# Kernel optimization log

Measured on AMD Instinct MI355X. Metric: run time of the kernel, lower is better.

Reference implementation:

```python
import jax, jax.numpy as jnp
import numpy as np

EPS = 1e-5  # torch InstanceNorm2d default eps


def setup_inputs() -> dict:
    key = jax.random.key(0)
    ks = jax.random.split(key, 5)
    B, C, H, W = 4, 64, 64, 64
    x = jax.random.normal(ks[0], (B, C, H, W), dtype=jnp.float32)
    # Conv2d 1x1 weights as [out_c, in_c] matrices (kernel dims squeezed)
    w_qkv = jax.random.normal(ks[1], (3 * C, C), dtype=jnp.float32) * (C ** -0.5)
    b_qkv = jax.random.normal(ks[2], (3 * C,), dtype=jnp.float32) * 0.02
    w_proj = jax.random.normal(ks[3], (C, C), dtype=jnp.float32) * (C ** -0.5)
    b_proj = jax.random.normal(ks[4], (C,), dtype=jnp.float32) * 0.02
    return {"x": x, "w_qkv": w_qkv, "b_qkv": b_qkv, "w_proj": w_proj, "b_proj": b_proj}


def reference(x, w_qkv, b_qkv, w_proj, b_proj):
    B, C, H, W = x.shape
    scale = C ** -0.5
    # InstanceNorm2d(affine=False): per-(B,C) stats over spatial dims, biased var
    mean = jnp.mean(x, axis=(2, 3), keepdims=True)
    var = jnp.var(x, axis=(2, 3), keepdims=True)
    h = (x - mean) * jax.lax.rsqrt(var + EPS)
    # 1x1 conv qkv projection: [B,3C,H,W]
    qkv = jnp.einsum('bchw,oc->bohw', h, w_qkv) + b_qkv[None, :, None, None]
    q, k, v = jnp.split(qkv, 3, axis=1)
    HW = H * W
    q = q.reshape(B, C, HW).transpose(0, 2, 1)  # [B, HW, C]
    k = k.reshape(B, C, HW)                      # [B, C, HW]
    v = v.reshape(B, C, HW).transpose(0, 2, 1)  # [B, HW, C]
    attn = jnp.einsum('bnc,bcm->bnm', q, k) * scale  # [B, HW, HW]
    attn = jax.nn.softmax(attn, axis=-1)
    # dropout p=0.0 -> identity
    h = jnp.einsum('bnm,bmc->bnc', attn, v)          # [B, HW, C]
    h = h.transpose(0, 2, 1).reshape(B, C, H, W)
    h = jnp.einsum('bchw,oc->bohw', h, w_proj) + b_proj[None, :, None, None]
    return x + h
```

## Files before the change

kernel.cpp:

```cpp
#include <hip/hip_runtime.h>
#include <hip/hip_bf16.h>

#define B_ 4
#define C_ 64
#define N_ 4096
#define EPS_ 1e-5f
#define C2_ 0.18033688011112042f

typedef __hip_bfloat16 bf16;
typedef __attribute__((ext_vector_type(8))) short short8;
typedef __attribute__((ext_vector_type(4))) short short4v;
typedef __attribute__((ext_vector_type(4))) float f32x4;

__device__ __forceinline__ float b2f(bf16 v) { return __bfloat162float(v); }

__device__ __forceinline__ short f2bs(float f) {
  union { bf16 h; short s; } u;
  u.h = __float2bfloat16(f);
  return u.s;
}

__device__ __forceinline__ short8 pk8(const float* f) {
  union { short8 v; short s[8]; } u;
#pragma unroll
  for (int i = 0; i < 8; ++i) u.s[i] = f2bs(f[i]);
  return u.v;
}

__device__ __forceinline__ void up8(short8 v, float* d) {
  union { short8 v; unsigned u[4]; } x;
  x.v = v;
  d[0] = __uint_as_float(x.u[0] << 16);
  d[1] = __uint_as_float(x.u[0] & 0xffff0000u);
  d[2] = __uint_as_float(x.u[1] << 16);
  d[3] = __uint_as_float(x.u[1] & 0xffff0000u);
  d[4] = __uint_as_float(x.u[2] << 16);
  d[5] = __uint_as_float(x.u[2] & 0xffff0000u);
  d[6] = __uint_as_float(x.u[3] << 16);
  d[7] = __uint_as_float(x.u[3] & 0xffff0000u);
}

template <bool F32>
__device__ __forceinline__ float ldx(const void* p, size_t idx) {
  if (F32) return ((const float*)p)[idx];
  return b2f(((const bf16*)p)[idx]);
}

template <bool F32>
__device__ __forceinline__ short8 ld8(const void* p, int idx) {
  if (F32) {
    const float* fp = (const float*)p + idx;
    float tmp[8];
    *(float4*)&tmp[0] = *(const float4*)fp;
    *(float4*)&tmp[4] = *(const float4*)(fp + 4);
    return pk8(tmp);
  }
  return *(const short8*)((const bf16*)p + idx);
}

__device__ __forceinline__ f32x4 mfma32(short8 a, short8 b, f32x4 c) {
  return __builtin_amdgcn_mfma_f32_16x16x32_bf16(a, b, c, 0, 0, 0);
}
__device__ __forceinline__ f32x4 mfma16(short4v a, short4v b, f32x4 c) {
  return __builtin_amdgcn_mfma_f32_16x16x16bf16_1k(a, b, c, 0, 0, 0);
}


template <bool F32>
__device__ __forceinline__ void stats_sum(const void* x, int bc, int t,
                                          float& s, float& s2) {
  if (F32) {
    const float4* xp = (const float4*)((const float*)x + (size_t)bc * N_);
#pragma unroll
    for (int r = 0; r < 4; ++r) {
      const float4 v = xp[r * 256 + t];
      s += (v.x + v.y) + (v.z + v.w);
      s2 += (v.x * v.x + v.y * v.y) + (v.z * v.z + v.w * v.w);
    }
  } else {
    const bf16* xp = (const bf16*)x + (size_t)bc * N_;
#pragma unroll
    for (int r = 0; r < 2; ++r) {
      float f[8];
      up8(*(const short8*)(xp + (r * 256 + t) * 8), f);
#pragma unroll
      for (int i = 0; i < 8; ++i) { s += f[i]; s2 += f[i] * f[i]; }
    }
  }
}

__global__ __launch_bounds__(256) void k_stats(const void* __restrict__ x,
                                               float* __restrict__ meanArr,
                                               float* __restrict__ rstdArr,
                                               int* __restrict__ flag) {
  const int bc = blockIdx.x, t = threadIdx.x;
  __shared__ float ps[4], ps2[4];
  __shared__ int pflag;
  {
    const ushort* xw = (const ushort*)x + (size_t)bc * 4096;
    int cnt = 0;
#pragma unroll
    for (int j = 0; j < 4; ++j) {
      const ushort4 u = *(const ushort4*)(xw + t * 16 + j * 4);
      cnt += ((u.x >> 7) & 0xFF) >= 143;
      cnt += ((u.y >> 7) & 0xFF) >= 143;
      cnt += ((u.z >> 7) & 0xFF) >= 143;
      cnt += ((u.w >> 7) & 0xFF) >= 143;
    }
#pragma unroll
    for (int off = 32; off > 0; off >>= 1) cnt += __shfl_down(cnt, off, 64);
    if (t == 0) pflag = 0;
    __syncthreads();
    if ((t & 63) == 0 && cnt > 16) atomicAdd(&pflag, cnt);
    __syncthreads();
  }
  const bool f32 = pflag > 64;
  float s = 0.f, s2 = 0.f;
  if (f32) stats_sum<true>(x, bc, t, s, s2);
  else stats_sum<false>(x, bc, t, s, s2);
#pragma unroll
  for (int off = 32; off > 0; off >>= 1) {
    s += __shfl_down(s, off, 64);
    s2 += __shfl_down(s2, off, 64);
  }
  if ((t & 63) == 0) { ps[t >> 6] = s; ps2[t >> 6] = s2; }
  __syncthreads();
  if (t == 0) {
    const float S = (ps[0] + ps[1]) + (ps[2] + ps[3]);
    const float S2 = (ps2[0] + ps2[1]) + (ps2[2] + ps2[3]);
    const float mean = S * (1.0f / N_);
    const float var = S2 * (1.0f / N_) - mean * mean;
    meanArr[bc] = mean;
    rstdArr[bc] = rsqrtf(var + EPS_);
    flag[0] = f32 ? 1 : 0;
  }
}

template <bool F32>
__device__ __forceinline__ void qkv_body(const void* x, const void* wqkv,
                                         const void* bqkv, const float* meanArr,
                                         const float* rstdArr, bf16* q, bf16* k,
                                         bf16* v, short* HB) {
  const int t = threadIdx.x, tj = blockIdx.x, b = blockIdx.y;
  const int n0 = tj * 64;
  {
    const int li = t & 15, nbt = (t >> 4) & 3, cg = t >> 6;
    const int n = n0 + nbt * 16 + li;
    const float* mb_ = meanArr + b * 64;
    const float* rb_ = rstdArr + b * 64;
    float hv[16];
#pragma unroll
    for (int i = 0; i < 16; ++i) {
      const int c = cg * 16 + i;
      hv[i] = (ldx<F32>(x, ((size_t)(b * 64 + c)) * N_ + n) - mb_[c]) * rb_[c];
    }
#pragma unroll
    for (int c8 = 0; c8 < 2; ++c8) {
      const int ks = cg >> 1, qd = (cg & 1) * 2 + c8;
      *(short8*)&HB[((nbt * 2 + ks) * 64 + qd * 16 + li) * 8] = pk8(&hv[c8 * 8]);
    }
  }
  __syncthreads();
  const int l = t & 63, w = t >> 6, li = l & 15, quad = l >> 4;
  short8 Wf[3][2];
#pragma unroll
  for (int sec = 0; sec < 3; ++sec)
#pragma unroll
    for (int ks = 0; ks < 2; ++ks)
      Wf[sec][ks] = ld8<F32>(wqkv, (sec * 64 + w * 16 + li) * 64 + ks * 32 + quad * 8);
  short8 Hf[4][2];
#pragma unroll
  for (int nb = 0; nb < 4; ++nb)
#pragma unroll
    for (int ks = 0; ks < 2; ++ks)
      Hf[nb][ks] = *(const short8*)&HB[((nb * 2 + ks) * 64 + l) * 8];
  float bq[4], bk[4];
#pragma unroll
  for (int r = 0; r < 4; ++r) {
    bq[r] = ldx<F32>(bqkv, w * 16 + quad * 4 + r);
    bk[r] = ldx<F32>(bqkv, 64 + w * 16 + quad * 4 + r);
  }
  const float bv = ldx<F32>(bqkv, 128 + w * 16 + li);
  const int lhi = ((w & 1) * 2 + (quad >> 1)) * 16 + li;
  const int jj0 = (quad & 1) * 4;
#pragma unroll
  for (int nb = 0; nb < 4; ++nb) {
    f32x4 dq = {0.f, 0.f, 0.f, 0.f}, dk = dq, dv = dq;
    dq = mfma32(Wf[0][0], Hf[nb][0], dq);
    dq = mfma32(Wf[0][1], Hf[nb][1], dq);
    dk = mfma32(Wf[1][0], Hf[nb][0], dk);
    dk = mfma32(Wf[1][1], Hf[nb][1], dk);
    dv = mfma32(Hf[nb][0], Wf[2][0], dv);
    dv = mfma32(Hf[nb][1], Wf[2][1], dv);
    union { ushort4 u; short s[4]; } pq, pk_, pv;
#pragma unroll
    for (int r = 0; r < 4; ++r) {
      pq.s[r] = f2bs(dq[r] + bq[r]);
      pk_.s[r] = f2bs(dk[r] + bk[r]);
      pv.s[r] = f2bs(dv[r] + bv);
    }
    *(ushort4*)&q[(((size_t)(b * 256 + tj * 4 + nb)) * 2 + (w >> 1)) * 512 + lhi * 8 + jj0] = pq.u;
    *(ushort4*)&k[(((size_t)(b * 64 + tj)) * 8 + nb * 2 + (w >> 1)) * 512 + lhi * 8 + jj0] = pk_.u;
    *(ushort4*)&v[(((size_t)(b * 64 + tj)) * 16 + w * 4 + nb) * 256 + (quad * 16 + li) * 4] = pv.u;
  }
}
__global__ __launch_bounds__(256) void k_qkv(
    const void* __restrict__ x, const void* __restrict__ wqkv,
    const void* __restrict__ bqkv, const float* __restrict__ meanArr,
    const float* __restrict__ rstdArr, bf16* __restrict__ q,
    bf16* __restrict__ k, bf16* __restrict__ v, const int* __restrict__ flag) {
  __shared__ short HB[4096];
  if (*flag) qkv_body<true>(x, wqkv, bqkv, meanArr, rstdArr, q, k, v, HB);
  else qkv_body<false>(x, wqkv, bqkv, meanArr, rstdArr, q, k, v, HB);
}

__global__ __launch_bounds__(256, 2) void k_attn(
    const bf16* __restrict__ qg, const bf16* __restrict__ kg,
    const bf16* __restrict__ vg, float* __restrict__ opart,
    float* __restrict__ lpart) {
  __shared__ float Oacc[64][68];
  __shared__ float lsum[4][64];
  const int bid = blockIdx.x;
  const int b = bid & 3, qt = (bid >> 2) & 63, kh = bid >> 8;
  const int t = threadIdx.x, l = t & 63, w = t >> 6, li = l & 15, quad = l >> 4;

  short8 Qf[4][2];
#pragma unroll
  for (int mb = 0; mb < 4; ++mb)
#pragma unroll
    for (int ks = 0; ks < 2; ++ks)
      Qf[mb][ks] = *(const short8*)(qg + (((size_t)(b * 256 + qt * 4 + mb)) * 2 + ks) * 512 + l * 8);

  f32x4 O[4][4];
#pragma unroll
  for (int cb = 0; cb < 4; ++cb)
#pragma unroll
    for (int mb = 0; mb < 4; ++mb) O[cb][mb] = {0.f, 0.f, 0.f, 0.f};
  float ls[4] = {0.f, 0.f, 0.f, 0.f};

  for (int it = 0; it < 8; ++it) {
    const int kt = kh * 32 + it * 4 + w;
    const size_t kb = ((size_t)(b * 64 + kt)) * 8 * 512;
    short8 Kf[4][2];
#pragma unroll
    for (int jb = 0; jb < 4; ++jb)
#pragma unroll
      for (int ks = 0; ks < 2; ++ks)
        Kf[jb][ks] = *(const short8*)(kg + kb + (jb * 2 + ks) * 512 + l * 8);
    const size_t vb = ((size_t)(b * 64 + kt)) * 16 * 256;
    short4v Vf[4][4];
#pragma unroll
    for (int cb = 0; cb < 4; ++cb)
#pragma unroll
      for (int jb = 0; jb < 4; ++jb)
        Vf[cb][jb] = *(const short4v*)(vg + vb + (cb * 4 + jb) * 256 + l * 4);
#pragma unroll
    for (int jb = 0; jb < 4; ++jb) {
      short4v Pf[4];
#pragma unroll
      for (int mb = 0; mb < 4; ++mb) {
        f32x4 s = {0.f, 0.f, 0.f, 0.f};
        s = mfma32(Kf[jb][0], Qf[mb][0], s);
        s = mfma32(Kf[jb][1], Qf[mb][1], s);
        const float p0 = exp2f(s[0] * C2_), p1 = exp2f(s[1] * C2_);
        const float p2 = exp2f(s[2] * C2_), p3 = exp2f(s[3] * C2_);
        ls[mb] += (p0 + p1) + (p2 + p3);
        union { short4v v; __hip_bfloat162 h[2]; } pu;
        pu.h[0] = __float22bfloat162_rn(make_float2(p0, p1));
        pu.h[1] = __float22bfloat162_rn(make_float2(p2, p3));
        Pf[mb] = pu.v;
      }
#pragma unroll
      for (int cb = 0; cb < 4; ++cb)
#pragma unroll
        for (int mb = 0; mb < 4; ++mb)
          O[cb][mb] = mfma16(Vf[cb][jb], Pf[mb], O[cb][mb]);
    }
  }
#pragma unroll
  for (int mb = 0; mb < 4; ++mb) {
    ls[mb] += __shfl_xor(ls[mb], 16, 64);
    ls[mb] += __shfl_xor(ls[mb], 32, 64);
  }
  if (l < 16) {
#pragma unroll
    for (int mb = 0; mb < 4; ++mb) lsum[w][mb * 16 + l] = ls[mb];
  }
  for (int ph = 0; ph < 4; ++ph) {
    if (w == ph) {
#pragma unroll
      for (int cb = 0; cb < 4; ++cb)
#pragma unroll
        for (int mb = 0; mb < 4; ++mb) {
          float4* dst = (float4*)&Oacc[mb * 16 + li][cb * 16 + quad * 4];
          float4 val;
          val.x = O[cb][mb][0]; val.y = O[cb][mb][1];
          val.z = O[cb][mb][2]; val.w = O[cb][mb][3];
          if (ph == 0) *dst = val;
          else {
            float4 cur = *dst;
            cur.x += val.x; cur.y += val.y; cur.z += val.z; cur.w += val.w;
            *dst = cur;
          }
        }
    }
    __syncthreads();
  }
  if (t < 64)
    lpart[(((size_t)(kh * 4 + b)) * 64 + qt) * 64 + t] =
        ((lsum[0][t] + lsum[1][t]) + (lsum[2][t] + lsum[3][t]));
  const size_t obase = (((size_t)(kh * 4 + b)) * 64 + qt) * 4096;
  const int m = t >> 2, cs = (t & 3) * 16;
#pragma unroll
  for (int k4 = 0; k4 < 4; ++k4)
    *(float4*)&opart[obase + m * 64 + cs + k4 * 4] =
        *(const float4*)&Oacc[m][cs + k4 * 4];
}

template <bool F32>
__device__ __forceinline__ void proj_body(const float* opart, const float* lpart,
                                          const void* xg, const void* wp,
                                          const void* bp, void* outv) {
  const int qt = blockIdx.x, b = blockIdx.y;
  const int t = threadIdx.x, l = t & 63, w = t >> 6, li = l & 15, quad = l >> 4;
  short8 Wa[2];
#pragma unroll
  for (int ks = 0; ks < 2; ++ks)
    Wa[ks] = ld8<F32>(wp, (w * 16 + li) * 64 + ks * 32 + quad * 8);
  const size_t ob0 = (((size_t)b) * 64 + qt) * 4096;
  const size_t ob1 = (((size_t)(4 + b)) * 64 + qt) * 4096;
  const size_t lb0 = (((size_t)b) * 64 + qt) * 64;
  const size_t lb1 = (((size_t)(4 + b)) * 64 + qt) * 64;
  float bpv[4];
#pragma unroll
  for (int r = 0; r < 4; ++r) bpv[r] = ldx<F32>(bp, w * 16 + quad * 4 + r);
  f32x4 D[4];
#pragma unroll
  for (int mb = 0; mb < 4; ++mb) {
    const int m = mb * 16 + li;
    const float lv = 1.0f / (lpart[lb0 + m] + lpart[lb1 + m]);
    f32x4 acc = {0.f, 0.f, 0.f, 0.f};
#pragma unroll
    for (int ks = 0; ks < 2; ++ks) {
      const int cb0 = ks * 32 + quad * 8;
      float s8[8];
      *(float4*)&s8[0] = *(const float4*)&opart[ob0 + m * 64 + cb0];
      *(float4*)&s8[4] = *(const float4*)&opart[ob0 + m * 64 + cb0 + 4];
      const float4 t1 = *(const float4*)&opart[ob1 + m * 64 + cb0];
      const float4 t2 = *(const float4*)&opart[ob1 + m * 64 + cb0 + 4];
      s8[0] += t1.x; s8[1] += t1.y; s8[2] += t1.z; s8[3] += t1.w;
      s8[4] += t2.x; s8[5] += t2.y; s8[6] += t2.z; s8[7] += t2.w;
#pragma unroll
      for (int i = 0; i < 8; ++i) s8[i] *= lv;
      acc = mfma32(Wa[ks], pk8(s8), acc);
    }
    D[mb] = acc;
  }
#pragma unroll
  for (int mb = 0; mb < 4; ++mb)
#pragma unroll
    for (int r = 0; r < 4; ++r) {
      const int o = w * 16 + quad * 4 + r;
      const int n = qt * 64 + mb * 16 + li;
      const size_t idx = ((size_t)(b * 64 + o)) * N_ + n;
      const float res = ldx<F32>(xg, idx) + D[mb][r] + bpv[r];
      if (F32) ((float*)outv)[idx] = res;
      else ((bf16*)outv)[idx] = __float2bfloat16(res);
    }
}
__global__ __launch_bounds__(256) void k_proj(
    const float* __restrict__ opart, const float* __restrict__ lpart,
    const void* __restrict__ xg, const void* __restrict__ wp,
    const void* __restrict__ bp, void* __restrict__ outv,
    const int* __restrict__ flag) {
  if (*flag) proj_body<true>(opart, lpart, xg, wp, bp, outv);
  else proj_body<false>(opart, lpart, xg, wp, bp, outv);
}

extern "C" void kernel_launch(void* const* d_in, const int* in_sizes, int n_in,
                              void* d_out, int out_size, void* d_ws,
                              size_t ws_size, hipStream_t stream) {
  const void* x = d_in[0];
  const void* wqkv = d_in[1];
  const void* bqkv = d_in[2];
  const void* wproj = d_in[3];
  const void* bproj = d_in[4];

  char* ws = (char*)d_ws;
  float* meanArr = (float*)ws;
  float* rstdArr = (float*)(ws + 1024);
  int* flag = (int*)(ws + 2048);
  bf16* q = (bf16*)(ws + 4096);
  bf16* k = (bf16*)(ws + 4096 + (2u << 20));
  bf16* v = (bf16*)(ws + 4096 + (4u << 20));
  float* opart = (float*)(ws + 4096 + (6u << 20));
  float* lpart = (float*)(ws + 4096 + (14u << 20));

  k_stats<<<256, 256, 0, stream>>>(x, meanArr, rstdArr, flag);
  k_qkv<<<dim3(64, 4), 256, 0, stream>>>(x, wqkv, bqkv, meanArr, rstdArr, q, k,
                                         v, flag);
  k_attn<<<512, 256, 0, stream>>>(q, k, v, opart, lpart);
  k_proj<<<dim3(64, 4), 256, 0, stream>>>(opart, lpart, x, wproj, bproj, d_out,
                                          flag);
}
```

Measured before the change: 120.9 us.

## Share K/V tiles across waves via LDS double-buffering and write bf16 partials

The attention kernel now has all four waves share each K/V tile, staged into double-buffered LDS with global_load_lds, while each wave owns a separate slice of queries. Before, each wave streamed its own K/V tile from global memory and the four waves' O were reduced through LDS. The key range is split four ways, with 128 queries per block. Partial outputs are stored as bf16 in MFMA fragment layout with no cross-wave reduction, and the projection kernel sums the four partials. This removes the LDS reduction and cuts global K/V traffic per query, at the cost of per-iteration barriers, extra bf16 rounding and more partial traffic into k_proj.

```diff
diff --git a/kernel.cpp b/kernel.cpp
--- a/kernel.cpp
+++ b/kernel.cpp
@@ -38,6 +38,13 @@
   d[5] = __uint_as_float(x.u[2] & 0xffff0000u);
   d[6] = __uint_as_float(x.u[3] << 16);
   d[7] = __uint_as_float(x.u[3] & 0xffff0000u);
+}
+
+__device__ __forceinline__ void up4(ushort4 u, float* d) {
+  d[0] = __uint_as_float(((unsigned)u.x) << 16);
+  d[1] = __uint_as_float(((unsigned)u.y) << 16);
+  d[2] = __uint_as_float(((unsigned)u.z) << 16);
+  d[3] = __uint_as_float(((unsigned)u.w) << 16);
 }
 
 template <bool F32>
@@ -214,142 +221,152 @@
   else qkv_body<false>(x, wqkv, bqkv, meanArr, rstdArr, q, k, v, HB);
 }
 
+__device__ __forceinline__ void stage(short* dst, const bf16* ks_,
+                                      const bf16* vs_, int w, int ln) {
+#pragma unroll
+  for (int i = 0; i < 2; ++i) {
+    const int off = w * 1024 + i * 512;
+    __builtin_amdgcn_global_load_lds(
+        (const __attribute__((address_space(1))) unsigned int*)(ks_ + off + ln * 8),
+        (__attribute__((address_space(3))) unsigned int*)(dst + off), 16, 0, 0);
+    __builtin_amdgcn_global_load_lds(
+        (const __attribute__((address_space(1))) unsigned int*)(vs_ + off + ln * 8),
+        (__attribute__((address_space(3))) unsigned int*)(dst + 4096 + off), 16, 0, 0);
+  }
+}
+
 __global__ __launch_bounds__(256, 2) void k_attn(
     const bf16* __restrict__ qg, const bf16* __restrict__ kg,
-    const bf16* __restrict__ vg, float* __restrict__ opart,
+    const bf16* __restrict__ vg, bf16* __restrict__ opart,
     float* __restrict__ lpart) {
-  __shared__ float Oacc[64][68];
-  __shared__ float lsum[4][64];
+  __shared__ __align__(16) short KV[2][8192];
   const int bid = blockIdx.x;
-  const int b = bid & 3, qt = (bid >> 2) & 63, kh = bid >> 8;
+  const int g = bid & 7, s = bid >> 3;
+  const int c = g * 2 + (s & 1);
+  const int b = c & 3, kh = c >> 2, qt = s >> 1;
   const int t = threadIdx.x, l = t & 63, w = t >> 6, li = l & 15, quad = l >> 4;
 
-  short8 Qf[4][2];
-#pragma unroll
-  for (int mb = 0; mb < 4; ++mb)
+  short8 Qf[2][2];
+#pragma unroll
+  for (int q = 0; q < 2; ++q)
 #pragma unroll
     for (int ks = 0; ks < 2; ++ks)
-      Qf[mb][ks] = *(const short8*)(qg + (((size_t)(b * 256 + qt * 4 + mb)) * 2 + ks) * 512 + l * 8);
-
-  f32x4 O[4][4];
+      Qf[q][ks] = *(const short8*)(qg +
+          (((size_t)(b * 256 + qt * 8 + w * 2 + q)) * 2 + ks) * 512 + l * 8);
+
+  f32x4 O[4][2];
 #pragma unroll
   for (int cb = 0; cb < 4; ++cb)
 #pragma unroll
-    for (int mb = 0; mb < 4; ++mb) O[cb][mb] = {0.f, 0.f, 0.f, 0.f};
-  float ls[4] = {0.f, 0.f, 0.f, 0.f};
-
-  for (int it = 0; it < 8; ++it) {
-    const int kt = kh * 32 + it * 4 + w;
-    const size_t kb = ((size_t)(b * 64 + kt)) * 8 * 512;
+    for (int q = 0; q < 2; ++q) O[cb][q] = {0.f, 0.f, 0.f, 0.f};
+  float ls[2] = {0.f, 0.f};
+
+  const bf16* kbase = kg + ((size_t)(b * 64 + kh * 16)) * 4096;
+  const bf16* vbase = vg + ((size_t)(b * 64 + kh * 16)) * 4096;
+
+  stage(&KV[0][0], kbase, vbase, w, l);
+  __syncthreads();
+  for (int it = 0; it < 16; ++it) {
+    const short* buf = &KV[it & 1][0];
+    if (it + 1 < 16)
+      stage(&KV[(it + 1) & 1][0], kbase + (size_t)(it + 1) * 4096,
+            vbase + (size_t)(it + 1) * 4096, w, l);
     short8 Kf[4][2];
 #pragma unroll
     for (int jb = 0; jb < 4; ++jb)
 #pragma unroll
       for (int ks = 0; ks < 2; ++ks)
-        Kf[jb][ks] = *(const short8*)(kg + kb + (jb * 2 + ks) * 512 + l * 8);
-    const size_t vb = ((size_t)(b * 64 + kt)) * 16 * 256;
+        Kf[jb][ks] = *(const short8*)&buf[(jb * 2 + ks) * 512 + l * 8];
     short4v Vf[4][4];
 #pragma unroll
     for (int cb = 0; cb < 4; ++cb)
 #pragma unroll
       for (int jb = 0; jb < 4; ++jb)
-        Vf[cb][jb] = *(const short4v*)(vg + vb + (cb * 4 + jb) * 256 + l * 4);
+        Vf[cb][jb] = *(const short4v*)&buf[4096 + (cb * 4 + jb) * 256 + l * 4];
 #pragma unroll
     for (int jb = 0; jb < 4; ++jb) {
-      short4v Pf[4];
-#pragma unroll
-      for (int mb = 0; mb < 4; ++mb) {
-        f32x4 s = {0.f, 0.f, 0.f, 0.f};
-        s = mfma32(Kf[jb][0], Qf[mb][0], s);
-        s = mfma32(Kf[jb][1], Qf[mb][1], s);
-        const float p0 = exp2f(s[0] * C2_), p1 = exp2f(s[1] * C2_);
-        const float p2 = exp2f(s[2] * C2_), p3 = exp2f(s[3] * C2_);
-        ls[mb] += (p0 + p1) + (p2 + p3);
+      short4v Pf[2];
+#pragma unroll
+      for (int q = 0; q < 2; ++q) {
+        f32x4 sv = {0.f, 0.f, 0.f, 0.f};
+        sv = mfma32(Kf[jb][0], Qf[q][0], sv);
+        sv = mfma32(Kf[jb][1], Qf[q][1], sv);
+        const float p0 = exp2f(sv[0] * C2_), p1 = exp2f(sv[1] * C2_);
+        const float p2 = exp2f(sv[2] * C2_), p3 = exp2f(sv[3] * C2_);
+        ls[q] += (p0 + p1) + (p2 + p3);
         union { short4v v; __hip_bfloat162 h[2]; } pu;
         pu.h[0] = __float22bfloat162_rn(make_float2(p0, p1));
         pu.h[1] = __float22bfloat162_rn(make_float2(p2, p3));
-        Pf[mb] = pu.v;
+        Pf[q] = pu.v;
       }
 #pragma unroll
       for (int cb = 0; cb < 4; ++cb)
 #pragma unroll
-        for (int mb = 0; mb < 4; ++mb)
-          O[cb][mb] = mfma16(Vf[cb][jb], Pf[mb], O[cb][mb]);
-    }
-  }
-#pragma unroll
-  for (int mb = 0; mb < 4; ++mb) {
-    ls[mb] += __shfl_xor(ls[mb], 16, 64);
-    ls[mb] += __shfl_xor(ls[mb], 32, 64);
-  }
+        for (int q = 0; q < 2; ++q)
+          O[cb][q] = mfma16(Vf[cb][jb], Pf[q], O[cb][q]);
+    }
+    __syncthreads();
+  }
+#pragma unroll
+  for (int q = 0; q < 2; ++q) {
+    ls[q] += __shfl_xor(ls[q], 16, 64);
+    ls[q] += __shfl_xor(ls[q], 32, 64);
+  }
+  const size_t pb = ((size_t)(kh * 4 + b)) * 32 + qt;
   if (l < 16) {
-#pragma unroll
-    for (int mb = 0; mb < 4; ++mb) lsum[w][mb * 16 + l] = ls[mb];
-  }
-  for (int ph = 0; ph < 4; ++ph) {
-    if (w == ph) {
-#pragma unroll
-      for (int cb = 0; cb < 4; ++cb)
-#pragma unroll
-        for (int mb = 0; mb < 4; ++mb) {
-          float4* dst = (float4*)&Oacc[mb * 16 + li][cb * 16 + quad * 4];
-          float4 val;
-          val.x = O[cb][mb][0]; val.y = O[cb][mb][1];
-          val.z = O[cb][mb][2]; val.w = O[cb][mb][3];
-          if (ph == 0) *dst = val;
-          else {
-            float4 cur = *dst;
-            cur.x += val.x; cur.y += val.y; cur.z += val.z; cur.w += val.w;
-            *dst = cur;
-          }
-        }
-    }
-    __syncthreads();
-  }
-  if (t < 64)
-    lpart[(((size_t)(kh * 4 + b)) * 64 + qt) * 64 + t] =
-        ((lsum[0][t] + lsum[1][t]) + (lsum[2][t] + lsum[3][t]));
-  const size_t obase = (((size_t)(kh * 4 + b)) * 64 + qt) * 4096;
-  const int m = t >> 2, cs = (t & 3) * 16;
-#pragma unroll
-  for (int k4 = 0; k4 < 4; ++k4)
-    *(float4*)&opart[obase + m * 64 + cs + k4 * 4] =
-        *(const float4*)&Oacc[m][cs + k4 * 4];
+    lpart[pb * 128 + (w * 2 + 0) * 16 + l] = ls[0];
+    lpart[pb * 128 + (w * 2 + 1) * 16 + l] = ls[1];
+  }
+#pragma unroll
+  for (int q = 0; q < 2; ++q)
+#pragma unroll
+    for (int cb = 0; cb < 4; ++cb) {
+      union { ushort4 u; short s[4]; } pk_;
+#pragma unroll
+      for (int r = 0; r < 4; ++r) pk_.s[r] = f2bs(O[cb][q][r]);
+      *(ushort4*)&opart[pb * 8192 + (((w * 2 + q) * 4 + cb) << 8) + l * 4] = pk_.u;
+    }
 }
 
 template <bool F32>
-__device__ __forceinline__ void proj_body(const float* opart, const float* lpart,
+__device__ __forceinline__ void proj_body(const bf16* opart, const float* lpart,
                                           const void* xg, const void* wp,
                                           const void* bp, void* outv) {
-  const int qt = blockIdx.x, b = blockIdx.y;
+  const int qt64 = blockIdx.x, bb = blockIdx.y;
+  const int qt = qt64 >> 1, mbo = (qt64 & 1) * 4;
   const int t = threadIdx.x, l = t & 63, w = t >> 6, li = l & 15, quad = l >> 4;
   short8 Wa[2];
 #pragma unroll
   for (int ks = 0; ks < 2; ++ks)
     Wa[ks] = ld8<F32>(wp, (w * 16 + li) * 64 + ks * 32 + quad * 8);
-  const size_t ob0 = (((size_t)b) * 64 + qt) * 4096;
-  const size_t ob1 = (((size_t)(4 + b)) * 64 + qt) * 4096;
-  const size_t lb0 = (((size_t)b) * 64 + qt) * 64;
-  const size_t lb1 = (((size_t)(4 + b)) * 64 + qt) * 64;
   float bpv[4];
 #pragma unroll
   for (int r = 0; r < 4; ++r) bpv[r] = ldx<F32>(bp, w * 16 + quad * 4 + r);
   f32x4 D[4];
 #pragma unroll
   for (int mb = 0; mb < 4; ++mb) {
-    const int m = mb * 16 + li;
-    const float lv = 1.0f / (lpart[lb0 + m] + lpart[lb1 + m]);
+    const int mbg = mbo + mb;
+    float lv = 0.f;
+#pragma unroll
+    for (int p = 0; p < 4; ++p)
+      lv += lpart[(((size_t)(p * 4 + bb)) * 32 + qt) * 128 + mbg * 16 + li];
+    lv = 1.0f / lv;
     f32x4 acc = {0.f, 0.f, 0.f, 0.f};
 #pragma unroll
     for (int ks = 0; ks < 2; ++ks) {
-      const int cb0 = ks * 32 + quad * 8;
-      float s8[8];
-      *(float4*)&s8[0] = *(const float4*)&opart[ob0 + m * 64 + cb0];
-      *(float4*)&s8[4] = *(const float4*)&opart[ob0 + m * 64 + cb0 + 4];
-      const float4 t1 = *(const float4*)&opart[ob1 + m * 64 + cb0];
-      const float4 t2 = *(const float4*)&opart[ob1 + m * 64 + cb0 + 4];
-      s8[0] += t1.x; s8[1] += t1.y; s8[2] += t1.z; s8[3] += t1.w;
-      s8[4] += t2.x; s8[5] += t2.y; s8[6] += t2.z; s8[7] += t2.w;
+      const int cb = ks * 2 + (quad >> 1);
+      const int qs0 = (quad & 1) * 2;
+      float s8[8] = {};
+#pragma unroll
+      for (int p = 0; p < 4; ++p) {
+        const size_t base =
+            (((size_t)(p * 4 + bb)) * 32 + qt) * 8192 + ((mbg * 4 + cb) << 8);
+        float f0[4], f1[4];
+        up4(*(const ushort4*)&opart[base + (qs0 * 16 + li) * 4], f0);
+        up4(*(const ushort4*)&opart[base + ((qs0 + 1) * 16 + li) * 4], f1);
+#pragma unroll
+        for (int i = 0; i < 4; ++i) { s8[i] += f0[i]; s8[4 + i] += f1[i]; }
+      }
 #pragma unroll
       for (int i = 0; i < 8; ++i) s8[i] *= lv;
       acc = mfma32(Wa[ks], pk8(s8), acc);
@@ -361,15 +378,15 @@
 #pragma unroll
     for (int r = 0; r < 4; ++r) {
       const int o = w * 16 + quad * 4 + r;
-      const int n = qt * 64 + mb * 16 + li;
-      const size_t idx = ((size_t)(b * 64 + o)) * N_ + n;
+      const int n = qt64 * 64 + mb * 16 + li;
+      const size_t idx = ((size_t)(bb * 64 + o)) * N_ + n;
       const float res = ldx<F32>(xg, idx) + D[mb][r] + bpv[r];
       if (F32) ((float*)outv)[idx] = res;
       else ((bf16*)outv)[idx] = __float2bfloat16(res);
     }
 }
 __global__ __launch_bounds__(256) void k_proj(
-    const float* __restrict__ opart, const float* __restrict__ lpart,
+    const bf16* __restrict__ opart, const float* __restrict__ lpart,
     const void* __restrict__ xg, const void* __restrict__ wp,
     const void* __restrict__ bp, void* __restrict__ outv,
     const int* __restrict__ flag) {
@@ -393,7 +410,7 @@
   bf16* q = (bf16*)(ws + 4096);
   bf16* k = (bf16*)(ws + 4096 + (2u << 20));
   bf16* v = (bf16*)(ws + 4096 + (4u << 20));
-  float* opart = (float*)(ws + 4096 + (6u << 20));
+  bf16* opart = (bf16*)(ws + 4096 + (6u << 20));
   float* lpart = (float*)(ws + 4096 + (14u << 20));
 
   k_stats<<<256, 256, 0, stream>>>(x, meanArr, rstdArr, flag);
```

Result: faster. 113.3 us (-6.3%).
